# Kernel optimization log

Hardware: AMD Instinct MI355X
Metric: run time of the kernel (lower is better)

## Reference

```python
import jax, jax.numpy as jnp
import numpy as np

EPSILON = 1e-6      # additive epsilon from the original module
COS_EPS = 1e-8      # torch cosine_similarity denominator clamp
MAX_SHIFT = 1       # shift kernel size = 2*MAX_SHIFT + 1


def setup_inputs() -> dict:
    key = jax.random.key(0)
    ks = jax.random.split(key, 7)
    B, N, F = 512, 2048, 128
    S = MAX_SHIFT
    return {
        "m": jax.random.normal(ks[0], (B, N, F), dtype=jnp.float32),        # memory
        "k": jax.random.normal(ks[1], (B, F), dtype=jnp.float32),           # key
        "b": jax.random.uniform(ks[2], (B, 1), dtype=jnp.float32) * 5.0,    # key strength (>0)
        "g": jax.random.uniform(ks[3], (B, 1), dtype=jnp.float32),          # interpolation gate in (0,1)
        "s": jax.nn.softmax(jax.random.normal(ks[4], (B, 2 * S + 1)), -1),  # shift distribution
        "r": 1.0 + jax.random.uniform(ks[5], (B, 1), dtype=jnp.float32),    # sharpening >= 1
        "w_prev": jax.nn.softmax(jax.random.normal(ks[6], (B, N)), -1),     # previous weight
    }


def reference(m, k, b, g, s, r, w_prev):
    # 1) content addressing: cosine similarity of (m + eps) rows vs (k + eps)
    me = m + EPSILON                       # [B, N, F]
    ke = k[:, None, :] + EPSILON           # [B, 1, F]
    num = jnp.einsum("bnf,bof->bn", me, ke)                       # [B, N]
    denom = jnp.linalg.norm(me, axis=-1) * jnp.linalg.norm(ke, axis=-1)
    sim = num / jnp.maximum(denom, COS_EPS)                       # [B, N]
    w = jax.nn.softmax(b * sim, axis=-1)                          # [B, N]

    # 2) interpolation with current position (faithful: w + (1-g)*w_prev)
    w = w + (1.0 - g) * w_prev

    # 3) circular shift: shifted[i] = sum_j s[j] * w[(i + j - S) mod N]
    S = MAX_SHIFT
    w = sum(s[:, j:j + 1] * jnp.roll(w, S - j, axis=1) for j in range(2 * S + 1))

    # 4) sharpen
    wr = w ** r
    return wr / (jnp.sum(wr, axis=1, keepdims=True) + EPSILON)
```

## Files before the change

### kernel.cpp

```cpp
#include <hip/hip_runtime.h>
#include <math.h>

#define EPSILON 1e-6f
#define COS_EPS 1e-8f
#define NN 2048
#define FF 128
#define BLK 512

__launch_bounds__(BLK, 2)
__global__ void ntm_head_kernel(const float* __restrict__ m,
                                const float* __restrict__ kk,
                                const float* __restrict__ beta_,
                                const float* __restrict__ g_,
                                const float* __restrict__ s_,
                                const float* __restrict__ r_,
                                const float* __restrict__ wp,
                                float* __restrict__ out) {
  const int b    = blockIdx.x;
  const int tid  = threadIdx.x;
  const int wv   = tid >> 6;
  const int lane = tid & 63;
  const int h    = lane >> 5;
  const int l32  = lane & 31;

  __shared__ float simbuf[NN];
  __shared__ float warr[NN];
  __shared__ float red[8];
  __shared__ float bc;

  const float beta = beta_[b];
  const float gg   = g_[b];
  const float s0 = s_[b * 3 + 0], s1 = s_[b * 3 + 1], s2 = s_[b * 3 + 2];
  const float rr = r_[b];

  float4 kv = *reinterpret_cast<const float4*>(kk + (size_t)b * FF + 4 * l32);
  const float ke0 = kv.x + EPSILON, ke1 = kv.y + EPSILON;
  const float ke2 = kv.z + EPSILON, ke3 = kv.w + EPSILON;
  float ksq = ke0 * ke0 + ke1 * ke1 + ke2 * ke2 + ke3 * ke3;
  #pragma unroll
  for (int off = 1; off < 32; off <<= 1) ksq += __shfl_xor(ksq, off);
  const float knorm = sqrtf(ksq);

  const float* mb = m + (size_t)b * NN * FF;

  float amax = -INFINITY;
  for (int it = 0; it < NN / 16; it += 4) {
    float4 mv[4];
    #pragma unroll
    for (int u = 0; u < 4; ++u) {
      int n = (it + u) * 16 + wv * 2 + h;
      mv[u] = *reinterpret_cast<const float4*>(mb + (size_t)n * FF + 4 * l32);
    }
    #pragma unroll
    for (int u = 0; u < 4; ++u) {
      int n = (it + u) * 16 + wv * 2 + h;
      float m0 = mv[u].x + EPSILON, m1 = mv[u].y + EPSILON;
      float m2 = mv[u].z + EPSILON, m3 = mv[u].w + EPSILON;
      float dp = m0 * ke0 + m1 * ke1 + m2 * ke2 + m3 * ke3;
      float sq = m0 * m0 + m1 * m1 + m2 * m2 + m3 * m3;
      #pragma unroll
      for (int off = 1; off < 32; off <<= 1) {
        dp += __shfl_xor(dp, off);
        sq += __shfl_xor(sq, off);
      }
      float a = beta * (dp / fmaxf(sqrtf(sq) * knorm, COS_EPS));
      if (l32 == 0) simbuf[n] = a;
      amax = fmaxf(amax, a);
    }
  }
  amax = fmaxf(amax, __shfl_xor(amax, 32));

  __syncthreads();
  if (lane == 0) red[wv] = amax;
  __syncthreads();
  if (tid == 0) {
    float v = red[0];
    #pragma unroll
    for (int i = 1; i < 8; ++i) v = fmaxf(v, red[i]);
    bc = v;
  }
  __syncthreads();
  const float amax_all = bc;

  float lsum = 0.f;
  #pragma unroll
  for (int i = 0; i < NN / BLK; ++i) {
    int n = tid + i * BLK;
    float e = expf(simbuf[n] - amax_all);
    simbuf[n] = e;
    lsum += e;
  }
  #pragma unroll
  for (int off = 1; off < 64; off <<= 1) lsum += __shfl_xor(lsum, off);
  __syncthreads();
  if (lane == 0) red[wv] = lsum;
  __syncthreads();
  if (tid == 0) {
    float v = 0.f;
    #pragma unroll
    for (int i = 0; i < 8; ++i) v += red[i];
    bc = v;
  }
  __syncthreads();
  const float inv_softmax = 1.0f / bc;
  const float om_g = 1.0f - gg;

  #pragma unroll
  for (int i = 0; i < NN / BLK; ++i) {
    int n = tid + i * BLK;
    warr[n] = simbuf[n] * inv_softmax + om_g * wp[(size_t)b * NN + n];
  }
  __syncthreads();

  float wrv[NN / BLK];
  float lsum2 = 0.f;
  #pragma unroll
  for (int i = 0; i < NN / BLK; ++i) {
    int n = tid + i * BLK;
    float prev = warr[(n + NN - 1) & (NN - 1)];
    float cur  = warr[n];
    float nxt  = warr[(n + 1) & (NN - 1)];
    float sh = s0 * prev + s1 * cur + s2 * nxt;
    float p = powf(sh, rr);
    wrv[i] = p;
    lsum2 += p;
  }
  #pragma unroll
  for (int off = 1; off < 64; off <<= 1) lsum2 += __shfl_xor(lsum2, off);
  __syncthreads();
  if (lane == 0) red[wv] = lsum2;
  __syncthreads();
  if (tid == 0) {
    float v = 0.f;
    #pragma unroll
    for (int i = 0; i < 8; ++i) v += red[i];
    bc = v;
  }
  __syncthreads();
  const float inv_sharp = 1.0f / (bc + EPSILON);

  #pragma unroll
  for (int i = 0; i < NN / BLK; ++i) {
    int n = tid + i * BLK;
    out[(size_t)b * NN + n] = wrv[i] * inv_sharp;
  }
}

extern "C" void kernel_launch(void* const* d_in, const int* in_sizes, int n_in,
                              void* d_out, int out_size, void* d_ws, size_t ws_size,
                              hipStream_t stream) {
  const float* m  = (const float*)d_in[0];
  const float* k  = (const float*)d_in[1];
  const float* b  = (const float*)d_in[2];
  const float* g  = (const float*)d_in[3];
  const float* s  = (const float*)d_in[4];
  const float* r  = (const float*)d_in[5];
  const float* wp = (const float*)d_in[6];
  float* out = (float*)d_out;

  ntm_head_kernel<<<dim3(512), dim3(BLK), 0, stream>>>(m, k, b, g, s, r, wp, out);
}
```

Measured before the change: 104.8 us.

## Fuse exp into the similarity pass and cut reduction barriers

Computes exp of the scaled cosine similarity directly inside the memory-streaming loop. This drops the max-subtraction pass and one block reduction, on the reasoning that beta times a cosine is bounded. It also deepens the load unroll from 4 to 8, preloads w_prev into registers at kernel start, and replaces sqrt/div/powf with rsq, __expf and __logf. Each reduction now has every thread read the per-wave partials, so there is no tid-0 broadcast and fewer __syncthreads. The trade-offs are possible overflow for large beta, the removed COS_EPS clamp, reduced numerical accuracy, and higher register pressure.

```diff
diff --git a/kernel.cpp b/kernel.cpp
--- a/kernel.cpp
+++ b/kernel.cpp
@@ -6,6 +6,7 @@
 #define NN 2048
 #define FF 128
 #define BLK 512
+#define UNROLL 8
 
 __launch_bounds__(BLK, 2)
 __global__ void ntm_head_kernel(const float* __restrict__ m,
@@ -25,8 +26,13 @@
 
   __shared__ float simbuf[NN];
   __shared__ float warr[NN];
-  __shared__ float red[8];
-  __shared__ float bc;
+  __shared__ float red_s[8];
+  __shared__ float red_p[8];
+
+  float wprv[NN / BLK];
+  #pragma unroll
+  for (int i = 0; i < NN / BLK; ++i)
+    wprv[i] = wp[(size_t)b * NN + tid + i * BLK];
 
   const float beta = beta_[b];
   const float gg   = g_[b];
@@ -39,20 +45,20 @@
   float ksq = ke0 * ke0 + ke1 * ke1 + ke2 * ke2 + ke3 * ke3;
   #pragma unroll
   for (int off = 1; off < 32; off <<= 1) ksq += __shfl_xor(ksq, off);
-  const float knorm = sqrtf(ksq);
+  const float inv_knorm = __builtin_amdgcn_rsqf(ksq);
 
   const float* mb = m + (size_t)b * NN * FF;
 
-  float amax = -INFINITY;
-  for (int it = 0; it < NN / 16; it += 4) {
-    float4 mv[4];
+  float lsum = 0.f;
+  for (int it = 0; it < NN / 16; it += UNROLL) {
+    float4 mv[UNROLL];
     #pragma unroll
-    for (int u = 0; u < 4; ++u) {
+    for (int u = 0; u < UNROLL; ++u) {
       int n = (it + u) * 16 + wv * 2 + h;
       mv[u] = *reinterpret_cast<const float4*>(mb + (size_t)n * FF + 4 * l32);
     }
     #pragma unroll
-    for (int u = 0; u < 4; ++u) {
+    for (int u = 0; u < UNROLL; ++u) {
       int n = (it + u) * 16 + wv * 2 + h;
       float m0 = mv[u].x + EPSILON, m1 = mv[u].y + EPSILON;
       float m2 = mv[u].z + EPSILON, m3 = mv[u].w + EPSILON;
@@ -63,52 +69,26 @@
         dp += __shfl_xor(dp, off);
         sq += __shfl_xor(sq, off);
       }
-      float a = beta * (dp / fmaxf(sqrtf(sq) * knorm, COS_EPS));
-      if (l32 == 0) simbuf[n] = a;
-      amax = fmaxf(amax, a);
+      float a = beta * dp * __builtin_amdgcn_rsqf(sq) * inv_knorm;
+      float e = __expf(a);
+      if (l32 == 0) simbuf[n] = e;
+      lsum += e;
     }
   }
-  amax = fmaxf(amax, __shfl_xor(amax, 32));
+  lsum += __shfl_xor(lsum, 32);
+  if (lane == 0) red_s[wv] = lsum;
+  __syncthreads();
 
-  __syncthreads();
-  if (lane == 0) red[wv] = amax;
-  __syncthreads();
-  if (tid == 0) {
-    float v = red[0];
-    #pragma unroll
-    for (int i = 1; i < 8; ++i) v = fmaxf(v, red[i]);
-    bc = v;
-  }
-  __syncthreads();
-  const float amax_all = bc;
-
-  float lsum = 0.f;
+  float ssum = 0.f;
   #pragma unroll
-  for (int i = 0; i < NN / BLK; ++i) {
-    int n = tid + i * BLK;
-    float e = expf(simbuf[n] - amax_all);
-    simbuf[n] = e;
-    lsum += e;
-  }
-  #pragma unroll
-  for (int off = 1; off < 64; off <<= 1) lsum += __shfl_xor(lsum, off);
-  __syncthreads();
-  if (lane == 0) red[wv] = lsum;
-  __syncthreads();
-  if (tid == 0) {
-    float v = 0.f;
-    #pragma unroll
-    for (int i = 0; i < 8; ++i) v += red[i];
-    bc = v;
-  }
-  __syncthreads();
-  const float inv_softmax = 1.0f / bc;
+  for (int i = 0; i < 8; ++i) ssum += red_s[i];
+  const float inv_softmax = 1.0f / ssum;
   const float om_g = 1.0f - gg;
 
   #pragma unroll
   for (int i = 0; i < NN / BLK; ++i) {
     int n = tid + i * BLK;
-    warr[n] = simbuf[n] * inv_softmax + om_g * wp[(size_t)b * NN + n];
+    warr[n] = simbuf[n] * inv_softmax + om_g * wprv[i];
   }
   __syncthreads();
 
@@ -121,23 +101,19 @@
     float cur  = warr[n];
     float nxt  = warr[(n + 1) & (NN - 1)];
     float sh = s0 * prev + s1 * cur + s2 * nxt;
-    float p = powf(sh, rr);
+    float p = __expf(rr * __logf(sh));
     wrv[i] = p;
     lsum2 += p;
   }
   #pragma unroll
   for (int off = 1; off < 64; off <<= 1) lsum2 += __shfl_xor(lsum2, off);
+  if (lane == 0) red_p[wv] = lsum2;
   __syncthreads();
-  if (lane == 0) red[wv] = lsum2;
-  __syncthreads();
-  if (tid == 0) {
-    float v = 0.f;
-    #pragma unroll
-    for (int i = 0; i < 8; ++i) v += red[i];
-    bc = v;
-  }
-  __syncthreads();
-  const float inv_sharp = 1.0f / (bc + EPSILON);
+
+  float psum = 0.f;
+  #pragma unroll
+  for (int i = 0; i < 8; ++i) psum += red_p[i];
+  const float inv_sharp = 1.0f / (psum + EPSILON);
 
   #pragma unroll
   for (int i = 0; i < NN / BLK; ++i) {
```

New measurement: 103.6 us. Within noise of the previous version (-1.1%).
